# Kernel optimization log

Hardware: AMD Instinct MI355X
Metric: run time of the kernel (lower is better)

## Reference

```python
import jax, jax.numpy as jnp
import numpy as np

# Production-scale dims: ViT patch attention on a 32x32 patch grid
B, L, F = 16, 1024, 512      # batch, seq (=NX*NY patches), model dim
H, D = 8, 64                 # heads, head_dim (F = H*D)
NX, NY = 32, 32              # patch grid; Toeplitz table size 4*NX*NY = 4096


def setup_inputs() -> dict:
    key = jax.random.key(0)
    ks = jax.random.split(key, 12)
    w = lambda k, shp: jax.random.normal(k, shp, jnp.float32) * 0.02
    return {
        "inputs_q": jax.random.normal(ks[0], (B, L, F), jnp.float32),
        "inputs_kv": jax.random.normal(ks[1], (B, L, F), jnp.float32),
        "Wq": w(ks[2], (F, H * D)), "bq": jnp.zeros((H * D,), jnp.float32),
        "Wk": w(ks[3], (F, H * D)), "bk": jnp.zeros((H * D,), jnp.float32),
        "Wv": w(ks[4], (F, H * D)), "bv": jnp.zeros((H * D,), jnp.float32),
        "Wo": w(ks[5], (H * D, F)), "bo": jnp.zeros((F,), jnp.float32),
        "toeplitz": w(ks[6], (H, 4 * NX * NY)),
    }


def _rel_index():
    # 2D relative-position (Toeplitz) index: patch p -> (x, y) on NX x NY grid.
    coords = jnp.arange(L)
    xi, yi = coords // NY, coords % NY
    dx = xi[:, None] - xi[None, :] + NX          # in [1, 2*NX-1]
    dy = yi[:, None] - yi[None, :] + NY          # in [1, 2*NY-1]
    return dx * (2 * NY) + dy                    # [L, L] indices into 4*NX*NY table


def reference(inputs_q, inputs_kv, Wq, bq, Wk, bk, Wv, bv, Wo, bo, toeplitz):
    q = (inputs_q @ Wq + bq).reshape(B, L, H, D)
    k = (inputs_kv @ Wk + bk).reshape(B, L, H, D)
    v = (inputs_kv @ Wv + bv).reshape(B, L, H, D)
    bias = toeplitz[:, _rel_index()]             # [H, L, L] Toeplitz relative bias
    scale = 1.0 / jnp.sqrt(jnp.float32(D))
    scores = jnp.einsum("bqhd,bkhd->bhqk", q, k) * scale + bias  # [B,H,L,L]
    attn = jax.nn.softmax(scores, axis=-1)
    x = jnp.einsum("bhqk,bkhd->bqhd", attn, v).reshape(B, L, H * D)
    out = x @ Wo + bo
    return out.reshape(B, L, H, D)               # matches torch forward's final reshape
```

## Files before the change

### kernel.cpp

```cpp
#include <hip/hip_runtime.h>
#include <hip/hip_bf16.h>

#define B_  16
#define L_  1024
#define F_  512
#define H_  8
#define D_  64
#define M_  (B_ * L_)
#define HD_ 512

typedef __bf16 bf16x8 __attribute__((ext_vector_type(8)));
typedef __bf16 bf16x4 __attribute__((ext_vector_type(4)));
typedef short  s16x4  __attribute__((ext_vector_type(4)));
typedef float  f32x4  __attribute__((ext_vector_type(4)));

__device__ __forceinline__ void gl_lds16(const void* g, void* l) {
  __builtin_amdgcn_global_load_lds(
      (const __attribute__((address_space(1))) unsigned int*)g,
      (__attribute__((address_space(3))) unsigned int*)l, 16, 0, 0);
}

__global__ __launch_bounds__(256) void wt_kernel(
    const float* __restrict__ Wq, const float* __restrict__ Wk,
    const float* __restrict__ Wv, const float* __restrict__ Wo,
    __bf16* __restrict__ Wt_all)
{
  const float* W = (blockIdx.z == 0) ? Wq : (blockIdx.z == 1) ? Wk
                 : (blockIdx.z == 2) ? Wv : Wo;
  __bf16* Wt = Wt_all + (size_t)blockIdx.z * (512 * 512);
  __shared__ float s[32][33];
  const int t = threadIdx.x;
  const int r = t >> 5, c = t & 31;
  const int k0 = blockIdx.x * 32, n0 = blockIdx.y * 32;
#pragma unroll
  for (int i = 0; i < 4; ++i)
    s[r + i * 8][c] = W[(size_t)(k0 + r + i * 8) * 512 + n0 + c];
  __syncthreads();
#pragma unroll
  for (int i = 0; i < 4; ++i)
    Wt[(size_t)(n0 + r + i * 8) * 512 + k0 + c] = (__bf16)s[c][r + i * 8];
}

__global__ __launch_bounds__(256) void cvt_kernel(
    const float* __restrict__ xq, const float* __restrict__ xkv,
    __bf16* __restrict__ oq, __bf16* __restrict__ okv)
{
  const float* src = blockIdx.y ? xkv : xq;
  __bf16* dst = blockIdx.y ? okv : oq;
  size_t i = ((size_t)blockIdx.x * 256 + threadIdx.x) * 8;
  float4 f0 = *(const float4*)(src + i);
  float4 f1 = *(const float4*)(src + i + 4);
  bf16x8 v;
  v[0] = (__bf16)f0.x; v[1] = (__bf16)f0.y; v[2] = (__bf16)f0.z; v[3] = (__bf16)f0.w;
  v[4] = (__bf16)f1.x; v[5] = (__bf16)f1.y; v[6] = (__bf16)f1.z; v[7] = (__bf16)f1.w;
  *(bf16x8*)(dst + i) = v;
}

__global__ __launch_bounds__(256) void gemm_proj_kernel(
    const __bf16* __restrict__ Xq, const __bf16* __restrict__ Xkv,
    const __bf16* __restrict__ Wt_all,
    const float* __restrict__ bq, const float* __restrict__ bk_,
    const float* __restrict__ bv_,
    __bf16* __restrict__ qd, __bf16* __restrict__ kd, __bf16* __restrict__ vd)
{
  const int seg = blockIdx.y >> 2;
  const __bf16* X = (seg == 0) ? Xq : Xkv;
  const __bf16* Wt = Wt_all + (size_t)seg * 262144;
  const float* bias = (seg == 0) ? bq : (seg == 1) ? bk_ : bv_;
  __bf16* dst = (seg == 0) ? qd : (seg == 1) ? kd : vd;
  const int mode = seg;

  __shared__ __align__(16) __bf16 As[4][128][8];
  __shared__ __align__(16) __bf16 Bs[4][128][8];
  const int t = threadIdx.x;
  const int m0 = blockIdx.x * 128, n0 = (blockIdx.y & 3) * 128;
  const int lane = t & 63, w = t >> 6;
  const int ml = lane & 15, quad = lane >> 4;
  const int wm = w & 1, wn = w >> 1;

  f32x4 acc[4][4];
#pragma unroll
  for (int i = 0; i < 4; ++i)
#pragma unroll
    for (int j = 0; j < 4; ++j) acc[i][j] = (f32x4){0.f, 0.f, 0.f, 0.f};

  for (int k0 = 0; k0 < 512; k0 += 32) {
    __syncthreads();
#pragma unroll
    for (int i = 0; i < 2; ++i) {
      int slot = (w + i * 4) * 64 + lane;
      int ko = slot >> 7, row = slot & 127;
      gl_lds16(&X[(size_t)(m0 + row) * 512 + k0 + ko * 8], &As[ko][row][0]);
      gl_lds16(&Wt[(size_t)(n0 + row) * 512 + k0 + ko * 8], &Bs[ko][row][0]);
    }
    __syncthreads();
    bf16x8 a[4], b[4];
#pragma unroll
    for (int mt = 0; mt < 4; ++mt)
      a[mt] = *(const bf16x8*)&As[quad][wm * 64 + mt * 16 + ml][0];
#pragma unroll
    for (int nt = 0; nt < 4; ++nt)
      b[nt] = *(const bf16x8*)&Bs[quad][wn * 64 + nt * 16 + ml][0];
#pragma unroll
    for (int mt = 0; mt < 4; ++mt)
#pragma unroll
      for (int nt = 0; nt < 4; ++nt)
        acc[mt][nt] =
            __builtin_amdgcn_mfma_f32_16x16x32_bf16(a[mt], b[nt], acc[mt][nt], 0, 0, 0);
  }

#pragma unroll
  for (int nt = 0; nt < 4; ++nt) {
    int col = n0 + wn * 64 + nt * 16 + ml;
    float bv = bias[col];
    int h = col >> 6, d = col & 63;
#pragma unroll
    for (int mt = 0; mt < 4; ++mt) {
      int row0 = m0 + wm * 64 + mt * 16 + quad * 4;
      int bz = row0 >> 10;
      int l0 = row0 & 1023;
      if (mode == 2) {
        bf16x4 pk;
#pragma unroll
        for (int r = 0; r < 4; ++r) pk[r] = (__bf16)(acc[mt][nt][r] + bv);
        size_t idx = ((size_t)(bz * H_ + h) * D_ + d) * L_ + l0;
        *(bf16x4*)&dst[idx] = pk;
      } else {
        size_t base = ((size_t)(bz * H_ + h) * L_ + l0) * D_ + d;
#pragma unroll
        for (int r = 0; r < 4; ++r)
          dst[base + (size_t)r * D_] = (__bf16)(acc[mt][nt][r] + bv);
      }
    }
  }
}

__global__ __launch_bounds__(256, 2) void attn_kernel(
    const __bf16* __restrict__ qg,
    const __bf16* __restrict__ kg,
    const __bf16* __restrict__ vg,
    const float* __restrict__ toep_g,
    __bf16* __restrict__ xg)
{
  __shared__ float toep[4096];
  __shared__ __align__(16) __bf16 Ks[2][64][64];
  __shared__ __align__(16) __bf16 Vs[2][64][64];

  const int t = threadIdx.x;
  const int n = blockIdx.x;
  const int bh = ((n >> 5) << 3) | (n & 7);
  const int q0 = ((n >> 3) & 3) * 256;
  const int h = bh & 7;
  const int lane = t & 63, w = t >> 6;
  const int ml = lane & 15, quad = lane >> 4;
  const int lo3 = lane >> 3;
  const int kop = lane & 7;

  const size_t qkbase = (size_t)bh * (L_ * D_);
  const size_t vbase  = (size_t)bh * (D_ * L_);

  {
    const float4* src = (const float4*)(toep_g + (size_t)h * 4096);
    float4* dl = (float4*)toep;
    for (int i = t; i < 1024; i += 256) dl[i] = src[i];
  }

#pragma unroll
  for (int i = 0; i < 2; ++i) {
    int row = (w * 2 + i) * 8 + lo3;
    int ko = kop ^ lo3;
    gl_lds16(&kg[qkbase + (size_t)row * D_ + ko * 8], &Ks[0][row][kop * 8]);
    gl_lds16(&vg[vbase + (size_t)row * L_ + ko * 8], &Vs[0][row][kop * 8]);
  }

  bf16x8 qf[4][2];
#pragma unroll
  for (int qn = 0; qn < 4; ++qn) {
    const __bf16* qp =
        qg + qkbase + (size_t)(q0 + w * 64 + qn * 16 + ml) * D_ + quad * 8;
    qf[qn][0] = *(const bf16x8*)qp;
    qf[qn][1] = *(const bf16x8*)(qp + 32);
  }

  float lpart[4] = {0.f, 0.f, 0.f, 0.f};
  f32x4 o[4][4];
#pragma unroll
  for (int qn = 0; qn < 4; ++qn)
#pragma unroll
    for (int dt = 0; dt < 4; ++dt) o[qn][dt] = (f32x4){0.f, 0.f, 0.f, 0.f};

  __syncthreads();

  int cur = 0;
  for (int k0 = 0; k0 < L_; k0 += 64) {
    if (k0 + 64 < L_) {
      int nb = cur ^ 1;
#pragma unroll
      for (int i = 0; i < 2; ++i) {
        int row = (w * 2 + i) * 8 + lo3;
        int ko = kop ^ lo3;
        gl_lds16(&kg[qkbase + (size_t)(k0 + 64 + row) * D_ + ko * 8],
                 &Ks[nb][row][kop * 8]);
        gl_lds16(&vg[vbase + (size_t)row * L_ + k0 + 64 + ko * 8],
                 &Vs[nb][row][kop * 8]);
      }
    }

#pragma unroll
    for (int nt = 0; nt < 4; ++nt) {
      bf16x8 kf0 = *(const bf16x8*)&Ks[cur][nt * 16 + ml][(quad ^ (ml & 7)) * 8];
      bf16x8 kf1 =
          *(const bf16x8*)&Ks[cur][nt * 16 + ml][((4 + quad) ^ (ml & 7)) * 8];
      int kx = (k0 >> 5) + (nt >> 1);

      s16x4 pfrag[4];
#pragma unroll
      for (int qn = 0; qn < 4; ++qn) {
        f32x4 z = (f32x4){0.f, 0.f, 0.f, 0.f};
        z = __builtin_amdgcn_mfma_f32_16x16x32_bf16(kf0, qf[qn][0], z, 0, 0, 0);
        z = __builtin_amdgcn_mfma_f32_16x16x32_bf16(kf1, qf[qn][1], z, 0, 0, 0);

        int qb = w * 64 + qn * 16;
        int base = (((q0 + qb) >> 5) - kx + 32) * 64 +
                   ((qb & 31) + ml - ((nt & 1) * 16 + quad * 4) + 32);
        float p[4];
#pragma unroll
        for (int r = 0; r < 4; ++r)
          p[r] = __expf(fmaf(z[r], 0.125f, toep[base - r]));
        lpart[qn] += (p[0] + p[1]) + (p[2] + p[3]);
        bf16x4 pk;
#pragma unroll
        for (int r = 0; r < 4; ++r) pk[r] = (__bf16)p[r];
        pfrag[qn] = __builtin_bit_cast(s16x4, pk);
      }

#pragma unroll
      for (int dt = 0; dt < 4; ++dt) {
        int row = dt * 16 + ml;
        int gc = nt * 2 + (quad >> 1);
        bf16x4 vfr = *(const bf16x4*)
            &Vs[cur][row][((gc ^ (row & 7)) * 8) + (quad & 1) * 4];
        s16x4 vfs = __builtin_bit_cast(s16x4, vfr);
#pragma unroll
        for (int qn = 0; qn < 4; ++qn)
          o[qn][dt] = __builtin_amdgcn_mfma_f32_16x16x16bf16_1k(
              pfrag[qn], vfs, o[qn][dt], 0, 0, 0);
      }
    }

    __syncthreads();
    cur ^= 1;
  }

#pragma unroll
  for (int qn = 0; qn < 4; ++qn) {
    lpart[qn] += __shfl_xor(lpart[qn], 16);
    lpart[qn] += __shfl_xor(lpart[qn], 32);
  }
  float linv[4][4];
#pragma unroll
  for (int qn = 0; qn < 4; ++qn)
#pragma unroll
    for (int r = 0; r < 4; ++r)
      linv[qn][r] = 1.0f / __shfl(lpart[qn], quad * 16 + quad * 4 + r);

#pragma unroll
  for (int qn = 0; qn < 4; ++qn)
#pragma unroll
    for (int dt = 0; dt < 4; ++dt)
#pragma unroll
      for (int r = 0; r < 4; ++r) {
        int row = q0 + w * 64 + qn * 16 + quad * 4 + r;
        xg[((size_t)(bh >> 3) * L_ + row) * 512 + h * 64 + dt * 16 + ml] =
            (__bf16)(o[qn][dt][r] * linv[qn][r]);
      }
}

__global__ __launch_bounds__(256) void gemm_out_kernel(
    const __bf16* __restrict__ Xb,
    const __bf16* __restrict__ Wt,
    const float* __restrict__ bo,
    float* __restrict__ out)
{
  __shared__ __align__(16) __bf16 As[4][128][8];
  __shared__ __align__(16) __bf16 Bs[4][128][8];
  const int t = threadIdx.x;
  const int m0 = blockIdx.x * 128, n0 = blockIdx.y * 128;
  const int lane = t & 63, w = t >> 6;
  const int ml = lane & 15, quad = lane >> 4;
  const int wm = w & 1, wn = w >> 1;

  f32x4 acc[4][4];
#pragma unroll
  for (int i = 0; i < 4; ++i)
#pragma unroll
    for (int j = 0; j < 4; ++j) acc[i][j] = (f32x4){0.f, 0.f, 0.f, 0.f};

  for (int k0 = 0; k0 < 512; k0 += 32) {
    __syncthreads();
#pragma unroll
    for (int i = 0; i < 2; ++i) {
      int slot = (w + i * 4) * 64 + lane;
      int ko = slot >> 7, row = slot & 127;
      gl_lds16(&Xb[(size_t)(m0 + row) * 512 + k0 + ko * 8], &As[ko][row][0]);
      gl_lds16(&Wt[(size_t)(n0 + row) * 512 + k0 + ko * 8], &Bs[ko][row][0]);
    }
    __syncthreads();
    bf16x8 a[4], b[4];
#pragma unroll
    for (int mt = 0; mt < 4; ++mt)
      a[mt] = *(const bf16x8*)&As[quad][wm * 64 + mt * 16 + ml][0];
#pragma unroll
    for (int nt = 0; nt < 4; ++nt)
      b[nt] = *(const bf16x8*)&Bs[quad][wn * 64 + nt * 16 + ml][0];
#pragma unroll
    for (int mt = 0; mt < 4; ++mt)
#pragma unroll
      for (int nt = 0; nt < 4; ++nt)
        acc[mt][nt] =
            __builtin_amdgcn_mfma_f32_16x16x32_bf16(a[mt], b[nt], acc[mt][nt], 0, 0, 0);
  }

#pragma unroll
  for (int nt = 0; nt < 4; ++nt) {
    int col = n0 + wn * 64 + nt * 16 + ml;
    float bv = bo[col];
#pragma unroll
    for (int mt = 0; mt < 4; ++mt) {
      int row0 = m0 + wm * 64 + mt * 16 + quad * 4;
#pragma unroll
      for (int r = 0; r < 4; ++r)
        out[(size_t)(row0 + r) * 512 + col] = acc[mt][nt][r] + bv;
    }
  }
}

extern "C" void kernel_launch(void* const* d_in, const int* in_sizes, int n_in,
                              void* d_out, int out_size, void* d_ws, size_t ws_size,
                              hipStream_t stream) {
  const float* inputs_q  = (const float*)d_in[0];
  const float* inputs_kv = (const float*)d_in[1];
  const float* Wq = (const float*)d_in[2];
  const float* bq = (const float*)d_in[3];
  const float* Wk = (const float*)d_in[4];
  const float* bk = (const float*)d_in[5];
  const float* Wv = (const float*)d_in[6];
  const float* bv = (const float*)d_in[7];
  const float* Wo = (const float*)d_in[8];
  const float* bo = (const float*)d_in[9];
  const float* toep = (const float*)d_in[10];
  float* out = (float*)d_out;

  char* ws = (char*)d_ws;
  __bf16* qb  = (__bf16*)(ws);
  __bf16* kb  = (__bf16*)(ws + 16777216);
  __bf16* vb  = (__bf16*)(ws + 33554432);
  __bf16* xb  = (__bf16*)(ws + 50331648);
  __bf16* Wt  = (__bf16*)(ws + 67108864);
  __bf16* xqb = (__bf16*)(ws + 69206016);
  __bf16* xkvb = xb;

  wt_kernel<<<dim3(16, 16, 4), 256, 0, stream>>>(Wq, Wk, Wv, Wo, Wt);
  cvt_kernel<<<dim3(4096, 2), 256, 0, stream>>>(inputs_q, inputs_kv, xqb, xkvb);
  gemm_proj_kernel<<<dim3(128, 12), 256, 0, stream>>>(
      xqb, xkvb, Wt, bq, bk, bv, qb, kb, vb);
  attn_kernel<<<dim3(512), 256, 0, stream>>>(qb, kb, vb, toep, xb);
  gemm_out_kernel<<<dim3(128, 4), 256, 0, stream>>>(xb, Wt + 3 * 262144, bo, out);
}
```

Baseline: 268.0 us.

## Double-buffer LDS tiles in projection and output GEMMs with async prefetch

Both bf16 GEMM kernels switch from a single LDS buffer to two. The next K-slice is issued via global_load_lds while the current slice feeds MFMAs, with manual s_waitcnt vmcnt(4) and barriers replacing the paired __syncthreads. Launch bounds also ask for 4 blocks per CU. This is meant to hide global-load latency behind compute, at the cost of twice the LDS per block and reliance on hand-written wait counts being correct.

```diff
diff --git a/kernel.cpp b/kernel.cpp
--- a/kernel.cpp
+++ b/kernel.cpp
@@ -56,7 +56,7 @@
   *(bf16x8*)(dst + i) = v;
 }
 
-__global__ __launch_bounds__(256) void gemm_proj_kernel(
+__global__ __launch_bounds__(256, 4) void gemm_proj_kernel(
     const __bf16* __restrict__ Xq, const __bf16* __restrict__ Xkv,
     const __bf16* __restrict__ Wt_all,
     const float* __restrict__ bq, const float* __restrict__ bk_,
@@ -70,8 +70,8 @@
   __bf16* dst = (seg == 0) ? qd : (seg == 1) ? kd : vd;
   const int mode = seg;
 
-  __shared__ __align__(16) __bf16 As[4][128][8];
-  __shared__ __align__(16) __bf16 Bs[4][128][8];
+  __shared__ __align__(16) __bf16 As[2][4][128][8];
+  __shared__ __align__(16) __bf16 Bs[2][4][128][8];
   const int t = threadIdx.x;
   const int m0 = blockIdx.x * 128, n0 = (blockIdx.y & 3) * 128;
   const int lane = t & 63, w = t >> 6;
@@ -84,30 +84,49 @@
 #pragma unroll
     for (int j = 0; j < 4; ++j) acc[i][j] = (f32x4){0.f, 0.f, 0.f, 0.f};
 
-  for (int k0 = 0; k0 < 512; k0 += 32) {
-    __syncthreads();
-#pragma unroll
-    for (int i = 0; i < 2; ++i) {
-      int slot = (w + i * 4) * 64 + lane;
-      int ko = slot >> 7, row = slot & 127;
-      gl_lds16(&X[(size_t)(m0 + row) * 512 + k0 + ko * 8], &As[ko][row][0]);
-      gl_lds16(&Wt[(size_t)(n0 + row) * 512 + k0 + ko * 8], &Bs[ko][row][0]);
-    }
-    __syncthreads();
-    bf16x8 a[4], b[4];
-#pragma unroll
-    for (int mt = 0; mt < 4; ++mt)
-      a[mt] = *(const bf16x8*)&As[quad][wm * 64 + mt * 16 + ml][0];
-#pragma unroll
-    for (int nt = 0; nt < 4; ++nt)
-      b[nt] = *(const bf16x8*)&Bs[quad][wn * 64 + nt * 16 + ml][0];
-#pragma unroll
-    for (int mt = 0; mt < 4; ++mt)
-#pragma unroll
-      for (int nt = 0; nt < 4; ++nt)
-        acc[mt][nt] =
-            __builtin_amdgcn_mfma_f32_16x16x32_bf16(a[mt], b[nt], acc[mt][nt], 0, 0, 0);
-  }
+  const int slot0 = w * 64 + lane;
+  const int slot1 = (w + 4) * 64 + lane;
+  const int ko0 = slot0 >> 7, row0_ = slot0 & 127;
+  const int ko1 = slot1 >> 7, row1_ = slot1 & 127;
+
+#define STAGE_PROJ(buf, kk)                                                     \
+  do {                                                                          \
+    gl_lds16(&X[(size_t)(m0 + row0_) * 512 + (kk) + ko0 * 8],                   \
+             &As[buf][ko0][row0_][0]);                                          \
+    gl_lds16(&Wt[(size_t)(n0 + row0_) * 512 + (kk) + ko0 * 8],                  \
+             &Bs[buf][ko0][row0_][0]);                                          \
+    gl_lds16(&X[(size_t)(m0 + row1_) * 512 + (kk) + ko1 * 8],                   \
+             &As[buf][ko1][row1_][0]);                                          \
+    gl_lds16(&Wt[(size_t)(n0 + row1_) * 512 + (kk) + ko1 * 8],                  \
+             &Bs[buf][ko1][row1_][0]);                                          \
+  } while (0)
+
+#define COMPUTE_TILE(buf)                                                       \
+  do {                                                                          \
+    bf16x8 a[4], b[4];                                                          \
+    _Pragma("unroll") for (int mt = 0; mt < 4; ++mt)                            \
+        a[mt] = *(const bf16x8*)&As[buf][quad][wm * 64 + mt * 16 + ml][0];      \
+    _Pragma("unroll") for (int nt = 0; nt < 4; ++nt)                            \
+        b[nt] = *(const bf16x8*)&Bs[buf][quad][wn * 64 + nt * 16 + ml][0];      \
+    _Pragma("unroll") for (int mt = 0; mt < 4; ++mt)                            \
+        _Pragma("unroll") for (int nt = 0; nt < 4; ++nt)                        \
+            acc[mt][nt] = __builtin_amdgcn_mfma_f32_16x16x32_bf16(              \
+                a[mt], b[nt], acc[mt][nt], 0, 0, 0);                            \
+  } while (0)
+
+  STAGE_PROJ(0, 0);
+#pragma unroll
+  for (int tt = 0; tt < 15; ++tt) {
+    const int cur = tt & 1;
+    STAGE_PROJ(cur ^ 1, (tt + 1) * 32);
+    asm volatile("s_waitcnt vmcnt(4)" ::: "memory");
+    asm volatile("s_barrier" ::: "memory");
+    COMPUTE_TILE(cur);
+    asm volatile("s_barrier" ::: "memory");
+  }
+  asm volatile("s_waitcnt vmcnt(0)" ::: "memory");
+  asm volatile("s_barrier" ::: "memory");
+  COMPUTE_TILE(1);
 
 #pragma unroll
   for (int nt = 0; nt < 4; ++nt) {
@@ -133,6 +152,8 @@
       }
     }
   }
+#undef STAGE_PROJ
+#undef COMPUTE_TILE
 }
 
 __global__ __launch_bounds__(256, 2) void attn_kernel(
@@ -276,14 +297,14 @@
       }
 }
 
-__global__ __launch_bounds__(256) void gemm_out_kernel(
+__global__ __launch_bounds__(256, 4) void gemm_out_kernel(
     const __bf16* __restrict__ Xb,
     const __bf16* __restrict__ Wt,
     const float* __restrict__ bo,
     float* __restrict__ out)
 {
-  __shared__ __align__(16) __bf16 As[4][128][8];
-  __shared__ __align__(16) __bf16 Bs[4][128][8];
+  __shared__ __align__(16) __bf16 As[2][4][128][8];
+  __shared__ __align__(16) __bf16 Bs[2][4][128][8];
   const int t = threadIdx.x;
   const int m0 = blockIdx.x * 128, n0 = blockIdx.y * 128;
   const int lane = t & 63, w = t >> 6;
@@ -296,30 +317,49 @@
 #pragma unroll
     for (int j = 0; j < 4; ++j) acc[i][j] = (f32x4){0.f, 0.f, 0.f, 0.f};
 
-  for (int k0 = 0; k0 < 512; k0 += 32) {
-    __syncthreads();
-#pragma unroll
-    for (int i = 0; i < 2; ++i) {
-      int slot = (w + i * 4) * 64 + lane;
-      int ko = slot >> 7, row = slot & 127;
-      gl_lds16(&Xb[(size_t)(m0 + row) * 512 + k0 + ko * 8], &As[ko][row][0]);
-      gl_lds16(&Wt[(size_t)(n0 + row) * 512 + k0 + ko * 8], &Bs[ko][row][0]);
-    }
-    __syncthreads();
-    bf16x8 a[4], b[4];
-#pragma unroll
-    for (int mt = 0; mt < 4; ++mt)
-      a[mt] = *(const bf16x8*)&As[quad][wm * 64 + mt * 16 + ml][0];
-#pragma unroll
-    for (int nt = 0; nt < 4; ++nt)
-      b[nt] = *(const bf16x8*)&Bs[quad][wn * 64 + nt * 16 + ml][0];
-#pragma unroll
-    for (int mt = 0; mt < 4; ++mt)
-#pragma unroll
-      for (int nt = 0; nt < 4; ++nt)
-        acc[mt][nt] =
-            __builtin_amdgcn_mfma_f32_16x16x32_bf16(a[mt], b[nt], acc[mt][nt], 0, 0, 0);
-  }
+  const int slot0 = w * 64 + lane;
+  const int slot1 = (w + 4) * 64 + lane;
+  const int ko0 = slot0 >> 7, row0_ = slot0 & 127;
+  const int ko1 = slot1 >> 7, row1_ = slot1 & 127;
+
+#define STAGE_OUT(buf, kk)                                                      \
+  do {                                                                          \
+    gl_lds16(&Xb[(size_t)(m0 + row0_) * 512 + (kk) + ko0 * 8],                  \
+             &As[buf][ko0][row0_][0]);                                          \
+    gl_lds16(&Wt[(size_t)(n0 + row0_) * 512 + (kk) + ko0 * 8],                  \
+             &Bs[buf][ko0][row0_][0]);                                          \
+    gl_lds16(&Xb[(size_t)(m0 + row1_) * 512 + (kk) + ko1 * 8],                  \
+             &As[buf][ko1][row1_][0]);                                          \
+    gl_lds16(&Wt[(size_t)(n0 + row1_) * 512 + (kk) + ko1 * 8],                  \
+             &Bs[buf][ko1][row1_][0]);                                          \
+  } while (0)
+
+#define COMPUTE_TILE_O(buf)                                                     \
+  do {                                                                          \
+    bf16x8 a[4], b[4];                                                          \
+    _Pragma("unroll") for (int mt = 0; mt < 4; ++mt)                            \
+        a[mt] = *(const bf16x8*)&As[buf][quad][wm * 64 + mt * 16 + ml][0];      \
+    _Pragma("unroll") for (int nt = 0; nt < 4; ++nt)                            \
+        b[nt] = *(const bf16x8*)&Bs[buf][quad][wn * 64 + nt * 16 + ml][0];      \
+    _Pragma("unroll") for (int mt = 0; mt < 4; ++mt)                            \
+        _Pragma("unroll") for (int nt = 0; nt < 4; ++nt)                        \
+            acc[mt][nt] = __builtin_amdgcn_mfma_f32_16x16x32_bf16(              \
+                a[mt], b[nt], acc[mt][nt], 0, 0, 0);                            \
+  } while (0)
+
+  STAGE_OUT(0, 0);
+#pragma unroll
+  for (int tt = 0; tt < 15; ++tt) {
+    const int cur = tt & 1;
+    STAGE_OUT(cur ^ 1, (tt + 1) * 32);
+    asm volatile("s_waitcnt vmcnt(4)" ::: "memory");
+    asm volatile("s_barrier" ::: "memory");
+    COMPUTE_TILE_O(cur);
+    asm volatile("s_barrier" ::: "memory");
+  }
+  asm volatile("s_waitcnt vmcnt(0)" ::: "memory");
+  asm volatile("s_barrier" ::: "memory");
+  COMPUTE_TILE_O(1);
 
 #pragma unroll
   for (int nt = 0; nt < 4; ++nt) {
@@ -333,6 +373,8 @@
         out[(size_t)(row0 + r) * 512 + col] = acc[mt][nt][r] + bv;
     }
   }
+#undef STAGE_OUT
+#undef COMPUTE_TILE_O
 }
 
 extern "C" void kernel_launch(void* const* d_in, const int* in_sizes, int n_in,
```

Measured after the change: 270.8 us. About the same (+1.0%).
